# Performance work log

Hardware: AMD Instinct MI355X
Metric: run time of the kernel (lower is better)

Reference implementation:

```python
import jax, jax.numpy as jnp
import numpy as np

N_NODES = 50000
IN_FEAT = 64
HIDDEN = 128
OUT = 10
N_EDGES = 800000


def setup_inputs() -> dict:
    key = jax.random.key(0)
    ks = jax.random.split(key, 8)
    s = lambda fan_in: 1.0 / np.sqrt(fan_in)
    x = jax.random.normal(ks[0], (N_NODES, IN_FEAT), dtype=jnp.float32)
    edge_index = jax.random.randint(ks[1], (2, N_EDGES), 0, N_NODES, dtype=jnp.int32)
    # SAGEConv params: lin_l (neighbor path, has bias) and lin_r (root path, no bias)
    W1l = jax.random.uniform(ks[2], (HIDDEN, IN_FEAT), jnp.float32, -s(IN_FEAT), s(IN_FEAT))
    b1 = jnp.zeros((HIDDEN,), jnp.float32)
    W1r = jax.random.uniform(ks[3], (HIDDEN, IN_FEAT), jnp.float32, -s(IN_FEAT), s(IN_FEAT))
    W2l = jax.random.uniform(ks[4], (OUT, HIDDEN), jnp.float32, -s(HIDDEN), s(HIDDEN))
    b2 = jnp.zeros((OUT,), jnp.float32)
    W2r = jax.random.uniform(ks[5], (OUT, HIDDEN), jnp.float32, -s(HIDDEN), s(HIDDEN))
    return {"x": x, "edge_index": edge_index, "W1l": W1l, "b1": b1, "W1r": W1r,
            "W2l": W2l, "b2": b2, "W2r": W2r}


def _sage_conv(x, src, dst, Wl, b, Wr, num_nodes):
    # mean-aggregate neighbor features (src -> dst), then linear + root linear
    msgs = x[src]                                                    # [E, d]
    agg = jax.ops.segment_sum(msgs, dst, num_segments=num_nodes)     # [N, d]
    cnt = jax.ops.segment_sum(jnp.ones((src.shape[0],), x.dtype), dst,
                              num_segments=num_nodes)                 # [N]
    mean = agg / jnp.maximum(cnt, 1.0)[:, None]
    return mean @ Wl.T + b + x @ Wr.T


def reference(x, edge_index, W1l, b1, W1r, W2l, b2, W2r):
    src, dst = edge_index[0], edge_index[1]
    n = x.shape[0]
    h = jax.nn.relu(_sage_conv(x, src, dst, W1l, b1, W1r, n))   # [N, hidden]
    h = _sage_conv(h, src, dst, W2l, b2, W2r, n)                 # [N, 10]
    # sum over nodes (transpose(0,1) then sum dim=1 == sum over axis 0)
    return jnp.sum(h, axis=0).reshape(1, OUT)
```

## Files before the change

### kernel.cpp

```cpp
#include <hip/hip_runtime.h>
#include <hip/hip_fp8.h>


constexpr int N = 50000;
constexpr int F = 64;
constexpr int H = 128;
constexpr int O = 10;
constexpr int E = 800000;

constexpr int NBUK = 391;
constexpr int CAPC = 2528;
constexpr int ADEPTH = 16;
constexpr int GSTR = 4;
constexpr int SPLIT = 8;
constexpr int NRED = 16;

constexpr int NTILE = (N + 63) / 64;

constexpr int GBIN_LEN  = NBUK * CAPC;
constexpr int GCUR_LEN  = NBUK * GSTR;
constexpr int RED_LEN   = NRED * 2 * H;
constexpr int ZLEN      = GCUR_LEN * 2 + RED_LEN;
constexpr int MEANH_LEN = N * F / 2;
constexpr int XQ_LEN    = N * F / 4;
constexpr size_t WS_NEED_Q =
    (size_t)GBIN_LEN * 2 + GCUR_LEN * 2 + RED_LEN + N + N + MEANH_LEN + XQ_LEN;

typedef _Float16 half2v __attribute__((ext_vector_type(2)));
typedef _Float16 f16x8 __attribute__((ext_vector_type(8)));
typedef float f32x4 __attribute__((ext_vector_type(4)));

__device__ __forceinline__ unsigned short f32_to_bf16_rne(float f) {
  unsigned u = __float_as_uint(f);
  u += 0x7FFFu + ((u >> 16) & 1u);
  return (unsigned short)(u >> 16);
}

__device__ __forceinline__ unsigned pack2h(float a, float b) {
  half2v h;
  h.x = (_Float16)a;
  h.y = (_Float16)b;
  return __builtin_bit_cast(unsigned, h);
}

__device__ __forceinline__ float fp8f(unsigned char b) {
  __hip_fp8_e4m3 t;
  t.__x = b;
  return (float)t;
}

__global__ __launch_bounds__(256) void k_cast(
    const float* __restrict__ x, unsigned* __restrict__ xq4,
    float* __restrict__ zbase, int do_cast) {
  const int tid = blockIdx.x * blockDim.x + threadIdx.x;
  if (tid < ZLEN) zbase[tid] = 0.0f;
  if (!do_cast) return;
  const int stride = gridDim.x * blockDim.x;
  for (int i = tid; i < N * F / 4; i += stride) {
    const float4 v = reinterpret_cast<const float4*>(x)[i];
    const __hip_fp8_e4m3 a(v.x), b(v.y), c(v.z), d(v.w);
    const unsigned o = (unsigned)a.__x | ((unsigned)b.__x << 8) |
                       ((unsigned)c.__x << 16) | ((unsigned)d.__x << 24);
    __builtin_nontemporal_store(o, xq4 + i);
  }
}

__global__ __launch_bounds__(256) void k_coarse(
    const int* __restrict__ ei, int* __restrict__ gcur,
    unsigned* __restrict__ gbin, int* __restrict__ gcur2,
    unsigned* __restrict__ gbin2) {
  __shared__ int scnt[NBUK];
  __shared__ unsigned stage[NBUK * ADEPTH];
  __shared__ int scnt2[NBUK];
  __shared__ unsigned stage2[NBUK * ADEPTH];
  const int tid = threadIdx.x;
  const int lane = tid & 63;
  const int wv = tid >> 6;
  for (int i = tid; i < NBUK; i += 256) { scnt[i] = 0; scnt2[i] = 0; }
  __syncthreads();

  const int chunk = E / 256;
  const int base = blockIdx.x * chunk;
  const int end = base + chunk;
  for (int e = base + tid; e < end; e += 256) {
    const int s = ei[e];
    const int d = ei[E + e];
    {
      const int b = d >> 7;
      const unsigned p = ((unsigned)s << 7) | (unsigned)(d & 127);
      const int pos = atomicAdd(&scnt[b], 1);
      if (pos < ADEPTH) {
        stage[b * ADEPTH + pos] = p;
      } else {
        const int g = atomicAdd(&gcur[b * GSTR], 1);
        if (g < CAPC) gbin[(size_t)b * CAPC + g] = p;
      }
    }
    {
      const int b2 = s >> 7;
      const unsigned p2 = ((unsigned)d << 7) | (unsigned)(s & 127);
      const int pos2 = atomicAdd(&scnt2[b2], 1);
      if (pos2 < ADEPTH) {
        stage2[b2 * ADEPTH + pos2] = p2;
      } else {
        const int g2 = atomicAdd(&gcur2[b2 * GSTR], 1);
        if (g2 < CAPC) gbin2[(size_t)b2 * CAPC + g2] = p2;
      }
    }
  }
  __syncthreads();

  for (int b0 = wv * 64 + lane; b0 < NBUK; b0 += 256) {
    int cnt = scnt[b0];
    if (cnt > ADEPTH) cnt = ADEPTH;
    if (cnt > 0) {
      const int gbase = atomicAdd(&gcur[b0 * GSTR], cnt);
      for (int k = 0; k < cnt; ++k) {
        const int g = gbase + k;
        if (g < CAPC) gbin[(size_t)b0 * CAPC + g] = stage[b0 * ADEPTH + k];
      }
    }
    int cnt2 = scnt2[b0];
    if (cnt2 > ADEPTH) cnt2 = ADEPTH;
    if (cnt2 > 0) {
      const int gbase2 = atomicAdd(&gcur2[b0 * GSTR], cnt2);
      for (int k = 0; k < cnt2; ++k) {
        const int g2 = gbase2 + k;
        if (g2 < CAPC) gbin2[(size_t)b0 * CAPC + g2] = stage2[b0 * ADEPTH + k];
      }
    }
  }
}

template <bool USE_Q>
__global__ __launch_bounds__(512) void k_agg2(
    const float* __restrict__ x, const unsigned char* __restrict__ xq,
    const int* __restrict__ gcur, const unsigned* __restrict__ gbin,
    unsigned short* __restrict__ mean1h, float* __restrict__ winv_g) {
  __shared__ int fcnt[16];
  __shared__ float winv_s[16];
  __shared__ unsigned short fbin[16][64];
  const int tid = threadIdx.x;
  const int lane = tid & 63;
  const int wv = __builtin_amdgcn_readfirstlane((int)(tid >> 6));
  const int b = blockIdx.x >> 3;
  const int part = blockIdx.x & 7;
  int mb = gcur[b * GSTR];
  if (mb > CAPC) mb = CAPC;

  if (tid < 16) fcnt[tid] = 0;
  __syncthreads();

  const unsigned* __restrict__ gb = gbin + (size_t)b * CAPC;
#define READF(I)                                                      \
  {                                                                   \
    unsigned P = 0;                                                   \
    const bool v = tid + (I) * 512 < mb;                              \
    if (v) P = gb[tid + (I) * 512];                                   \
    const int row = (int)(P & 127u);                                  \
    if (v && ((row >> 4) == part)) {                                  \
      const int dl = row & 15;                                        \
      const int pos = atomicAdd(&fcnt[dl], 1);                        \
      if (pos < 46) fbin[dl][pos] = (unsigned short)(P >> 7);         \
    }                                                                 \
  }
  READF(0) READF(1) READF(2) READF(3) READF(4)
#undef READF
  __syncthreads();

  if (tid < 16) {
    const int c = fcnt[tid];
    const float wv_ = 1.0f / (float)(c > 0 ? c : 1);
    winv_s[tid] = wv_;
    const int n = b * 128 + part * 16 + tid;
    if (n < N) winv_g[n] = wv_;
  }
  __syncthreads();

  #pragma unroll
  for (int r = 0; r < 2; ++r) {
    const int row = wv * 2 + r;
    const int n = b * 128 + part * 16 + row;
    if (n >= N) break;
    int m = __builtin_amdgcn_readfirstlane(fcnt[row]);
    const float winv = winv_s[row];
    if (m > 46) m = 46;
    const uint4* __restrict__ lq = reinterpret_cast<const uint4*>(&fbin[row][0]);
    const uint4 q0 = lq[0], q1 = lq[1], q2 = lq[2];
    const uint4 q3 = lq[3], q4 = lq[4], q5 = lq[5];
    float acc = 0.f;
#define DO2(U, base)                                                      \
    {                                                                     \
      const unsigned u = __builtin_amdgcn_readfirstlane(U);               \
      int sa = (int)(u & 0xFFFFu), sb = (int)(u >> 16);                   \
      sa = sa < N ? sa : 0;  sb = sb < N ? sb : 0;     \
      float va, vb;                                                      \
      if constexpr (USE_Q) {                                              \
        va = fp8f(xq[(size_t)sa * F + lane]);                             \
        vb = fp8f(xq[(size_t)sb * F + lane]);                             \
      } else {                                                            \
        va = x[(size_t)sa * F + lane];                                    \
        vb = x[(size_t)sb * F + lane];                                    \
      }                                                                   \
      acc += ((base) < m) ? va : 0.f;                                     \
      acc += ((base) + 1 < m) ? vb : 0.f;                                 \
    }
    if (m > 0)  { DO2(q0.x, 0)  DO2(q0.y, 2)  DO2(q0.z, 4)  DO2(q0.w, 6)  }
    if (m > 8)  { DO2(q1.x, 8)  DO2(q1.y, 10) DO2(q1.z, 12) DO2(q1.w, 14) }
    if (m > 16) { DO2(q2.x, 16) DO2(q2.y, 18) DO2(q2.z, 20) DO2(q2.w, 22) }
    if (m > 24) { DO2(q3.x, 24) DO2(q3.y, 26) DO2(q3.z, 28) DO2(q3.w, 30) }
    if (m > 32) { DO2(q4.x, 32) DO2(q4.y, 34) DO2(q4.z, 36) DO2(q4.w, 38) }
    if (m > 40) { DO2(q5.x, 40) DO2(q5.y, 42) DO2(q5.z, 44) }
#undef DO2
    mean1h[(size_t)n * F + lane] = f32_to_bf16_rne(acc * winv);
  }
}

__global__ __launch_bounds__(512) void k_wsum(
    const int* __restrict__ gcur2, const unsigned* __restrict__ gbin2,
    const float* __restrict__ winv_g, float* __restrict__ wsum) {
  __shared__ float lsum[128];
  const int tid = threadIdx.x;
  const int b = blockIdx.x;
  int mb = gcur2[b * GSTR];
  if (mb > CAPC) mb = CAPC;
  if (tid < 128) lsum[tid] = 0.f;
  __syncthreads();
  const unsigned* __restrict__ gb = gbin2 + (size_t)b * CAPC;
  #pragma unroll
  for (int i = 0; i < 5; ++i) {
    const int idx = tid + i * 512;
    if (idx < mb) {
      const unsigned p = gb[idx];
      atomicAdd(&lsum[p & 127u], winv_g[p >> 7]);
    }
  }
  __syncthreads();
  const int n = b * 128 + tid;
  if (tid < 128 && n < N) wsum[n] = lsum[tid];
}

template <bool USE_Q>
__global__ __launch_bounds__(256) void k_trans(
    const float* __restrict__ x, const unsigned char* __restrict__ xq,
    const unsigned short* __restrict__ mean1h,
    const float* __restrict__ wsum,
    const float* __restrict__ W1l, const float* __restrict__ b1,
    const float* __restrict__ W1r,
    float* __restrict__ Sred) {
  __shared__ unsigned short swt[128 * 128];
  __shared__ unsigned short sfeat[64 * 128];
  const int tid = threadIdx.x;
  const int nbase = blockIdx.x * 64;
  const int lane = tid & 63;
  const int wv = tid >> 6;
  const int lrow = lane & 15;
  const int lgrp = lane >> 4;

  #pragma unroll
  for (int u = 0; u < 16; ++u) {
    const int idx = u * 256 + tid;
    const int j = idx >> 5;
    const int q = idx & 31;
    const float4 v = (q < 16)
        ? *reinterpret_cast<const float4*>(&W1l[j * F + q * 4])
        : *reinterpret_cast<const float4*>(&W1r[j * F + (q - 16) * 4]);
    const unsigned p01 = pack2h(v.x, v.y);
    const unsigned p23 = pack2h(v.z, v.w);
    ushort4 o;
    o.x = (unsigned short)(p01 & 0xFFFFu);
    o.y = (unsigned short)(p01 >> 16);
    o.z = (unsigned short)(p23 & 0xFFFFu);
    o.w = (unsigned short)(p23 >> 16);
    const int qs = (((q >> 1) ^ (j & 15)) << 1) | (q & 1);
    *reinterpret_cast<ushort4*>(&swt[j * 128 + qs * 4]) = o;
  }

  #pragma unroll
  for (int u = 0; u < 8; ++u) {
    const int idx = u * 256 + tid;
    const int nn = idx >> 5;
    const int q = idx & 31;
    const int gn = nbase + nn;
    ushort4 o;
    o.x = 0; o.y = 0; o.z = 0; o.w = 0;
    if (gn < N) {
      float f0, f1, f2, f3;
      if (q < 16) {
        const ushort4 t4 = reinterpret_cast<const ushort4*>(mean1h + (size_t)gn * F)[q];
        f0 = __uint_as_float((unsigned)t4.x << 16);
        f1 = __uint_as_float((unsigned)t4.y << 16);
        f2 = __uint_as_float((unsigned)t4.z << 16);
        f3 = __uint_as_float((unsigned)t4.w << 16);
      } else if constexpr (USE_Q) {
        const unsigned qq = *reinterpret_cast<const unsigned*>(
            xq + (size_t)gn * F + (q - 16) * 4);
        f0 = fp8f((unsigned char)(qq & 0xFFu));
        f1 = fp8f((unsigned char)((qq >> 8) & 0xFFu));
        f2 = fp8f((unsigned char)((qq >> 16) & 0xFFu));
        f3 = fp8f((unsigned char)(qq >> 24));
      } else {
        const float4 v = reinterpret_cast<const float4*>(x + (size_t)gn * F)[q - 16];
        f0 = v.x; f1 = v.y; f2 = v.z; f3 = v.w;
      }
      const unsigned p01 = pack2h(f0, f1);
      const unsigned p23 = pack2h(f2, f3);
      o.x = (unsigned short)(p01 & 0xFFFFu);
      o.y = (unsigned short)(p01 >> 16);
      o.z = (unsigned short)(p23 & 0xFFFFu);
      o.w = (unsigned short)(p23 >> 16);
    }
    const int qs = (((q >> 1) ^ (nn & 15)) << 1) | (q & 1);
    *reinterpret_cast<ushort4*>(&sfeat[nn * 128 + qs * 4]) = o;
  }
  __syncthreads();

  f16x8 A[4];
  #pragma unroll
  for (int kc = 0; kc < 4; ++kc) {
    const int row = wv * 16 + lrow;
    const int u16 = (kc * 4 + lgrp) ^ lrow;
    A[kc] = *reinterpret_cast<const f16x8*>(&sfeat[row * 128 + u16 * 8]);
  }

  f32x4 acc[8];
  #pragma unroll
  for (int js = 0; js < 8; ++js) acc[js] = (f32x4){0.f, 0.f, 0.f, 0.f};
  #pragma unroll
  for (int js = 0; js < 8; ++js) {
    #pragma unroll
    for (int kc = 0; kc < 4; ++kc) {
      const int jr = js * 16 + lrow;
      const int u16 = (kc * 4 + lgrp) ^ lrow;
      const f16x8 B = *reinterpret_cast<const f16x8*>(&swt[jr * 128 + u16 * 8]);
      acc[js] = __builtin_amdgcn_mfma_f32_16x16x32_f16(A[kc], B, acc[js], 0, 0, 0);
    }
  }

  float wsn[4];
  bool vld[4];
  const int node0 = nbase + wv * 16 + lgrp * 4;
  #pragma unroll
  for (int reg = 0; reg < 4; ++reg) {
    vld[reg] = (node0 + reg) < N;
    wsn[reg] = vld[reg] ? wsum[node0 + reg] : 0.f;
  }
  float sS[8], sW[8];
  #pragma unroll
  for (int js = 0; js < 8; ++js) {
    const float bj = b1[js * 16 + lrow];
    float s = 0.f, w = 0.f;
    #pragma unroll
    for (int reg = 0; reg < 4; ++reg) {
      const float h = vld[reg] ? fmaxf(acc[js][reg] + bj, 0.f) : 0.f;
      s += h;
      w = fmaf(wsn[reg], h, w);
    }
    s += __shfl_xor(s, 16, 64); s += __shfl_xor(s, 32, 64);
    w += __shfl_xor(w, 16, 64); w += __shfl_xor(w, 32, 64);
    sS[js] = s; sW[js] = w;
  }

  __syncthreads();
  float* redS = reinterpret_cast<float*>(sfeat);
  float* redW = reinterpret_cast<float*>(sfeat) + 512;
  if (lgrp == 0) {
    #pragma unroll
    for (int js = 0; js < 8; ++js) {
      redS[wv * 128 + js * 16 + lrow] = sS[js];
      redW[wv * 128 + js * 16 + lrow] = sW[js];
    }
  }
  __syncthreads();
  if (tid < 128) {
    const int c = blockIdx.x & (NRED - 1);
    float s = redS[tid] + redS[128 + tid] + redS[256 + tid] + redS[384 + tid];
    float w = redW[tid] + redW[128 + tid] + redW[256 + tid] + redW[384 + tid];
    atomicAdd(&Sred[c * 256 + tid], s);
    atomicAdd(&Sred[c * 256 + 128 + tid], w);
  }
}

__global__ __launch_bounds__(64) void k_final(
    const float* __restrict__ Sred,
    const float* __restrict__ W2l, const float* __restrict__ b2,
    const float* __restrict__ W2r, float* __restrict__ out) {
  const int j = threadIdx.x;
  if (j < O) {
    float acc = (float)N * b2[j];
    for (int k = 0; k < H; ++k) {
      float sh = 0.f, sw = 0.f;
      #pragma unroll
      for (int c = 0; c < NRED; ++c) {
        sh += Sred[c * 256 + k];
        sw += Sred[c * 256 + 128 + k];
      }
      acc += sw * W2l[j * H + k] + sh * W2r[j * H + k];
    }
    out[j] = acc;
  }
}

extern "C" void kernel_launch(void* const* d_in, const int* in_sizes, int n_in,
                              void* d_out, int out_size, void* d_ws, size_t ws_size,
                              hipStream_t stream) {
  const float* x   = (const float*)d_in[0];
  const int*   ei  = (const int*)d_in[1];
  const float* W1l = (const float*)d_in[2];
  const float* b1  = (const float*)d_in[3];
  const float* W1r = (const float*)d_in[4];
  const float* W2l = (const float*)d_in[5];
  const float* b2  = (const float*)d_in[6];
  const float* W2r = (const float*)d_in[7];
  float* out = (float*)d_out;
  float* ws  = (float*)d_ws;

  const bool use_q = ws_size >= WS_NEED_Q * 4;

  size_t off = 0;
  unsigned* gbin = (unsigned*)ws; off += GBIN_LEN;
  unsigned* gbin2 = (unsigned*)(ws + off); off += GBIN_LEN;
  int* gcur = (int*)(ws + off); off += GCUR_LEN;
  int* gcur2 = (int*)(ws + off); off += GCUR_LEN;
  float* Sred = ws + off; off += RED_LEN;
  float* winv_g = ws + off; off += N;
  float* wsum = ws + off; off += N;
  unsigned short* mean1h = (unsigned short*)(ws + off); off += MEANH_LEN;
  unsigned char* xq = nullptr;
  if (use_q) { xq = (unsigned char*)(ws + off); off += XQ_LEN; }

  hipLaunchKernelGGL(k_cast, dim3(512), dim3(256), 0, stream,
                     x, (unsigned*)xq, (float*)gcur, use_q ? 1 : 0);
  hipLaunchKernelGGL(k_coarse, dim3(256), dim3(256), 0, stream,
                     ei, gcur, gbin, gcur2, gbin2);
  if (use_q) {
    hipLaunchKernelGGL(k_agg2<true>, dim3(NBUK * SPLIT), dim3(512), 0, stream,
                       x, xq, gcur, gbin, mean1h, winv_g);
  } else {
    hipLaunchKernelGGL(k_agg2<false>, dim3(NBUK * SPLIT), dim3(512), 0, stream,
                       x, xq, gcur, gbin, mean1h, winv_g);
  }
  hipLaunchKernelGGL(k_wsum, dim3(NBUK), dim3(512), 0, stream,
                     gcur2, gbin2, winv_g, wsum);
  if (use_q) {
    hipLaunchKernelGGL(k_trans<true>, dim3(NTILE), dim3(256), 0, stream,
                       x, xq, mean1h, wsum, W1l, b1, W1r, Sred);
  } else {
    hipLaunchKernelGGL(k_trans<false>, dim3(NTILE), dim3(256), 0, stream,
                       x, xq, mean1h, wsum, W1l, b1, W1r, Sred);
  }
  hipLaunchKernelGGL(k_final, dim3(1), dim3(64), 0, stream,
                     Sred, W2l, b2, W2r, out);
}
```

Before: 117.6 us.

## Fuse weighted-sum scatter into transform kernel with 128-node tiles

Merges the k_wsum kernel (LDS-atomic accumulation of per-node inverse-degree weights from the second edge bin) into the MFMA transform kernel. Each block now covers 128 nodes with 512 threads, matching the bucket size, so the weights stay in shared memory. This removes one kernel launch and the global wsum buffer round-trip. In exchange it doubles shared memory per block and halves the number of blocks (391 versus 782), which may reduce occupancy and latency hiding.

```diff
diff --git a/kernel.cpp b/kernel.cpp
--- a/kernel.cpp
+++ b/kernel.cpp
@@ -14,8 +14,6 @@
 constexpr int GSTR = 4;
 constexpr int SPLIT = 8;
 constexpr int NRED = 16;
-
-constexpr int NTILE = (N + 63) / 64;
 
 constexpr int GBIN_LEN  = NBUK * CAPC;
 constexpr int GCUR_LEN  = NBUK * GSTR;
@@ -24,7 +22,7 @@
 constexpr int MEANH_LEN = N * F / 2;
 constexpr int XQ_LEN    = N * F / 4;
 constexpr size_t WS_NEED_Q =
-    (size_t)GBIN_LEN * 2 + GCUR_LEN * 2 + RED_LEN + N + N + MEANH_LEN + XQ_LEN;
+    (size_t)GBIN_LEN * 2 + GCUR_LEN * 2 + RED_LEN + N + MEANH_LEN + XQ_LEN;
 
 typedef _Float16 half2v __attribute__((ext_vector_type(2)));
 typedef _Float16 f16x8 __attribute__((ext_vector_type(8)));
@@ -216,50 +214,44 @@
   }
 }
 
-__global__ __launch_bounds__(512) void k_wsum(
+template <bool USE_Q>
+__global__ __launch_bounds__(512) void k_wt(
+    const float* __restrict__ x, const unsigned char* __restrict__ xq,
     const int* __restrict__ gcur2, const unsigned* __restrict__ gbin2,
-    const float* __restrict__ winv_g, float* __restrict__ wsum) {
-  __shared__ float lsum[128];
-  const int tid = threadIdx.x;
-  const int b = blockIdx.x;
-  int mb = gcur2[b * GSTR];
-  if (mb > CAPC) mb = CAPC;
-  if (tid < 128) lsum[tid] = 0.f;
-  __syncthreads();
-  const unsigned* __restrict__ gb = gbin2 + (size_t)b * CAPC;
-  #pragma unroll
-  for (int i = 0; i < 5; ++i) {
-    const int idx = tid + i * 512;
-    if (idx < mb) {
-      const unsigned p = gb[idx];
-      atomicAdd(&lsum[p & 127u], winv_g[p >> 7]);
-    }
-  }
-  __syncthreads();
-  const int n = b * 128 + tid;
-  if (tid < 128 && n < N) wsum[n] = lsum[tid];
-}
-
-template <bool USE_Q>
-__global__ __launch_bounds__(256) void k_trans(
-    const float* __restrict__ x, const unsigned char* __restrict__ xq,
+    const float* __restrict__ winv_g,
     const unsigned short* __restrict__ mean1h,
-    const float* __restrict__ wsum,
     const float* __restrict__ W1l, const float* __restrict__ b1,
     const float* __restrict__ W1r,
     float* __restrict__ Sred) {
   __shared__ unsigned short swt[128 * 128];
-  __shared__ unsigned short sfeat[64 * 128];
+  __shared__ unsigned short sfeat[128 * 128];
+  __shared__ float lsum[128];
   const int tid = threadIdx.x;
-  const int nbase = blockIdx.x * 64;
+  const int b = blockIdx.x;
+  const int nbase = b * 128;
   const int lane = tid & 63;
   const int wv = tid >> 6;
   const int lrow = lane & 15;
   const int lgrp = lane >> 4;
 
-  #pragma unroll
-  for (int u = 0; u < 16; ++u) {
-    const int idx = u * 256 + tid;
+  if (tid < 128) lsum[tid] = 0.f;
+  __syncthreads();
+
+  int mb = gcur2[b * GSTR];
+  if (mb > CAPC) mb = CAPC;
+  const unsigned* __restrict__ g2 = gbin2 + (size_t)b * CAPC;
+  #pragma unroll
+  for (int i = 0; i < 5; ++i) {
+    const int idx = tid + i * 512;
+    if (idx < mb) {
+      const unsigned p = g2[idx];
+      atomicAdd(&lsum[p & 127u], winv_g[p >> 7]);
+    }
+  }
+
+  #pragma unroll
+  for (int u = 0; u < 8; ++u) {
+    const int idx = u * 512 + tid;
     const int j = idx >> 5;
     const int q = idx & 31;
     const float4 v = (q < 16)
@@ -278,7 +270,7 @@
 
   #pragma unroll
   for (int u = 0; u < 8; ++u) {
-    const int idx = u * 256 + tid;
+    const int idx = u * 512 + tid;
     const int nn = idx >> 5;
     const int q = idx & 31;
     const int gn = nbase + nn;
@@ -339,11 +331,11 @@
 
   float wsn[4];
   bool vld[4];
-  const int node0 = nbase + wv * 16 + lgrp * 4;
+  const int r0 = wv * 16 + lgrp * 4;
   #pragma unroll
   for (int reg = 0; reg < 4; ++reg) {
-    vld[reg] = (node0 + reg) < N;
-    wsn[reg] = vld[reg] ? wsum[node0 + reg] : 0.f;
+    vld[reg] = (nbase + r0 + reg) < N;
+    wsn[reg] = lsum[r0 + reg];
   }
   float sS[8], sW[8];
   #pragma unroll
@@ -363,7 +355,7 @@
 
   __syncthreads();
   float* redS = reinterpret_cast<float*>(sfeat);
-  float* redW = reinterpret_cast<float*>(sfeat) + 512;
+  float* redW = reinterpret_cast<float*>(sfeat) + 1024;
   if (lgrp == 0) {
     #pragma unroll
     for (int js = 0; js < 8; ++js) {
@@ -373,9 +365,13 @@
   }
   __syncthreads();
   if (tid < 128) {
-    const int c = blockIdx.x & (NRED - 1);
-    float s = redS[tid] + redS[128 + tid] + redS[256 + tid] + redS[384 + tid];
-    float w = redW[tid] + redW[128 + tid] + redW[256 + tid] + redW[384 + tid];
+    float s = 0.f, w = 0.f;
+    #pragma unroll
+    for (int m = 0; m < 8; ++m) {
+      s += redS[m * 128 + tid];
+      w += redW[m * 128 + tid];
+    }
+    const int c = b & (NRED - 1);
     atomicAdd(&Sred[c * 256 + tid], s);
     atomicAdd(&Sred[c * 256 + 128 + tid], w);
   }
@@ -424,7 +420,6 @@
   int* gcur2 = (int*)(ws + off); off += GCUR_LEN;
   float* Sred = ws + off; off += RED_LEN;
   float* winv_g = ws + off; off += N;
-  float* wsum = ws + off; off += N;
   unsigned short* mean1h = (unsigned short*)(ws + off); off += MEANH_LEN;
   unsigned char* xq = nullptr;
   if (use_q) { xq = (unsigned char*)(ws + off); off += XQ_LEN; }
@@ -436,18 +431,13 @@
   if (use_q) {
     hipLaunchKernelGGL(k_agg2<true>, dim3(NBUK * SPLIT), dim3(512), 0, stream,
                        x, xq, gcur, gbin, mean1h, winv_g);
+    hipLaunchKernelGGL(k_wt<true>, dim3(NBUK), dim3(512), 0, stream,
+                       x, xq, gcur2, gbin2, winv_g, mean1h, W1l, b1, W1r, Sred);
   } else {
     hipLaunchKernelGGL(k_agg2<false>, dim3(NBUK * SPLIT), dim3(512), 0, stream,
                        x, xq, gcur, gbin, mean1h, winv_g);
-  }
-  hipLaunchKernelGGL(k_wsum, dim3(NBUK), dim3(512), 0, stream,
-                     gcur2, gbin2, winv_g, wsum);
-  if (use_q) {
-    hipLaunchKernelGGL(k_trans<true>, dim3(NTILE), dim3(256), 0, stream,
-                       x, xq, mean1h, wsum, W1l, b1, W1r, Sred);
-  } else {
-    hipLaunchKernelGGL(k_trans<false>, dim3(NTILE), dim3(256), 0, stream,
-                       x, xq, mean1h, wsum, W1l, b1, W1r, Sred);
+    hipLaunchKernelGGL(k_wt<false>, dim3(NBUK), dim3(512), 0, stream,
+                       x, xq, gcur2, gbin2, winv_g, mean1h, W1l, b1, W1r, Sred);
   }
   hipLaunchKernelGGL(k_final, dim3(1), dim3(64), 0, stream,
                      Sred, W2l, b2, W2r, out);
```

Result: faster. 109.2 us (median of 2 runs) (-7.1%).
